# Optimization experiments

Measured on AMD Instinct MI355X. Metric: run time of the kernel, lower is better.

Reference implementation:

```python
import jax, jax.numpy as jnp
import numpy as np

N_QUBITS = 10
N_LAYERS = 4
BATCH = 2048


def setup_inputs() -> dict:
    key = jax.random.key(0)
    k1, k2 = jax.random.split(key)
    x = jax.random.normal(k1, (BATCH, N_QUBITS), dtype=jnp.float32)
    q_params = jax.random.normal(k2, (N_LAYERS * N_QUBITS * 3,), dtype=jnp.float32) * 0.01
    return {"x": x, "q_params": q_params}


def _apply_1q(state, U, wire):
    # state: (B, 2, 2, ..., 2); U: (2, 2) complex. Applies U on `wire`.
    s = jnp.moveaxis(state, wire + 1, -1)
    s = jnp.einsum('...j,ij->...i', s, U)
    return jnp.moveaxis(s, -1, wire + 1)


def _apply_cnot(state, ctrl, tgt):
    # flip target amplitude pair where control bit == 1
    s = jnp.moveaxis(state, (ctrl + 1, tgt + 1), (-2, -1))
    s = jnp.concatenate([s[..., 0:1, :], s[..., 1:2, ::-1]], axis=-2)
    return jnp.moveaxis(s, (-2, -1), (ctrl + 1, tgt + 1))


def _forward(x, q_params):
    B = x.shape[0]
    n, L = N_QUBITS, N_LAYERS
    # --- data-encoding layer: RY(x_i)|0> = [cos(x_i/2), sin(x_i/2)] per qubit ---
    half = 0.5 * x
    amps = jnp.stack([jnp.cos(half), jnp.sin(half)], axis=-1).astype(jnp.complex64)  # (B, n, 2)
    state = amps[:, 0, :]
    for i in range(1, n):  # build product state via successive kron (loop over n_qubits only)
        state = (state[:, :, None] * amps[:, i, None, :]).reshape(B, -1)
    state = state.reshape((B,) + (2,) * n)
    # --- variational gate matrices: per (layer, qubit) fused U = RZ @ RY @ RX ---
    w = q_params.reshape(L, n, 3)
    c, s = jnp.cos(0.5 * w), jnp.sin(0.5 * w)
    cx = c[..., 0].astype(jnp.complex64); sx = s[..., 0].astype(jnp.complex64)
    cy = c[..., 1].astype(jnp.complex64); sy = s[..., 1].astype(jnp.complex64)
    ez = jnp.exp(-0.5j * w[..., 2].astype(jnp.complex64))
    zeros = jnp.zeros_like(ez)
    Urx = jnp.stack([jnp.stack([cx, -1j * sx], -1), jnp.stack([-1j * sx, cx], -1)], -2)  # (L,n,2,2)
    Ury = jnp.stack([jnp.stack([cy, -sy], -1), jnp.stack([sy, cy], -1)], -2)
    Urz = jnp.stack([jnp.stack([ez, zeros], -1), jnp.stack([zeros, jnp.conj(ez)], -1)], -2)
    U = jnp.einsum('lnab,lnbc,lncd->lnad', Urz, Ury, Urx)  # apply order: RX then RY then RZ
    # --- circuit layers ---
    for l in range(L):
        for i in range(n):
            state = _apply_1q(state, U[l, i], i)
        for i in range(n - 1):
            state = _apply_cnot(state, i, i + 1)
    # --- <Z_i> expectation values ---
    p = jnp.abs(state) ** 2  # (B, 2, ..., 2) real probabilities
    evs = []
    for i in range(n):
        axes = tuple(a for a in range(1, n + 1) if a != i + 1)
        pi = jnp.sum(p, axis=axes)  # (B, 2)
        evs.append(pi[:, 0] - pi[:, 1])
    return jnp.stack(evs, axis=-1)  # (B, n_qubits)


def reference(x, q_params):
    return _forward(x, q_params)
```

## Files before the change

### kernel.cpp

```cpp
#include <hip/hip_runtime.h>
#include <math.h>

#define NQ 10
#define NL 4
#define NGATES (NL * NQ)
#define NTHREADS 256
#define WPB 4

typedef float f32x2 __attribute__((ext_vector_type(2)));

#if __has_builtin(__builtin_amdgcn_permlane32_swap)
#define HAVE_PLSWAP 1
#else
#define HAVE_PLSWAP 0
#endif


template<int XM>
__device__ __forceinline__ float exch1(float v, bool selP) {
    if constexpr (XM == 0) return v;
    int x = __float_as_int(v);
    constexpr int low = XM & 31;
    if constexpr (low == 1)      x = __builtin_amdgcn_mov_dpp(x, 0xB1, 0xF, 0xF, true);
    else if constexpr (low == 2) x = __builtin_amdgcn_mov_dpp(x, 0x4E, 0xF, 0xF, true);
    else if constexpr (low == 3) x = __builtin_amdgcn_mov_dpp(x, 0x1B, 0xF, 0xF, true);
    else if constexpr (low != 0) x = __builtin_amdgcn_ds_swizzle(x, (low << 10) | 0x1F);
    if constexpr ((XM & 32) != 0) {
#if HAVE_PLSWAP
        auto r = __builtin_amdgcn_permlane32_swap((unsigned)x, (unsigned)x, false, false);
        x = selP ? (int)r[0] : (int)r[1];
#else
        x = __float_as_int(__shfl_xor(__int_as_float(x), 32, 64));
#endif
    }
    return __int_as_float(x);
}

template<int XM>
__device__ __forceinline__ f32x2 exch2(f32x2 v, bool selP) {
    f32x2 r;
    r.x = exch1<XM>(v.x, selP);
    r.y = exch1<XM>(v.y, selP);
    return r;
}

__device__ __forceinline__ f32x2 cfma4(f32x2 A, f32x2 st, f32x2 B, f32x2 pst) {
    f32x2 t;
    asm("v_pk_mul_f32 %0, %1, %2 op_sel:[0,0] op_sel_hi:[0,1]\n\t"
        "v_pk_fma_f32 %0, %1, %2, %0 op_sel:[1,1,0] op_sel_hi:[1,0,1] neg_lo:[0,1,0]\n\t"
        "v_pk_fma_f32 %0, %3, %4, %0 op_sel:[0,0,0] op_sel_hi:[0,1,1]\n\t"
        "v_pk_fma_f32 %0, %3, %4, %0 op_sel:[1,1,0] op_sel_hi:[1,0,1] neg_lo:[0,1,0]"
        : "=&v"(t)
        : "v"(A), "v"(st), "v"(B), "v"(pst));
    return t;
}

template<int XM, int XR, int SL, int SR>
__device__ __forceinline__ void gate(f32x2 (&st)[16], const f32x2* g4,
                                     int lane, bool selP) {
    f32x2 u00 = g4[0], u01 = g4[1], u10 = g4[2], u11 = g4[3];
    bool hl = (__popc(lane & SL) & 1) != 0;
    f32x2 A0, B0, A1, B1;
    A0.x = hl ? u11.x : u00.x;  A0.y = hl ? u11.y : u00.y;
    B0.x = hl ? u10.x : u01.x;  B0.y = hl ? u10.y : u01.y;
    A1.x = hl ? u00.x : u11.x;  A1.y = hl ? u00.y : u11.y;
    B1.x = hl ? u01.x : u10.x;  B1.y = hl ? u01.y : u10.y;
    f32x2 pst[16];
    #pragma unroll
    for (int r = 0; r < 16; ++r) pst[r] = exch2<XM>(st[r ^ XR], selP);
    #pragma unroll
    for (int r = 0; r < 16; ++r) {
        const bool p1 = (__builtin_popcount(r & SR) & 1) != 0;
        f32x2 Ar = p1 ? A1 : A0;
        f32x2 Br = p1 ? B1 : B0;
        st[r] = cfma4(Ar, st[r], Br, pst[r]);
    }
}

__device__ __forceinline__ float wht6(float v, int lane, bool selP) {
    float t;
    t = exch1<1>(v, selP);   v = (lane & 1)  ? (t - v) : (v + t);
    t = exch1<2>(v, selP);   v = (lane & 2)  ? (t - v) : (v + t);
    t = exch1<4>(v, selP);   v = (lane & 4)  ? (t - v) : (v + t);
    t = exch1<8>(v, selP);   v = (lane & 8)  ? (t - v) : (v + t);
    t = exch1<16>(v, selP);  v = (lane & 16) ? (t - v) : (v + t);
    t = exch1<32>(v, selP);  v = (lane & 32) ? (t - v) : (v + t);
    return v;
}

__global__ __launch_bounds__(NTHREADS, 2) void qlayer_kernel(
    const float* __restrict__ x,
    const float* __restrict__ qp,
    float* __restrict__ out,
    int B)
{
    __shared__ f32x2 su[NGATES][4];

    const int t = threadIdx.x;
    if (t < NGATES) {
        float w0 = qp[t * 3 + 0], w1 = qp[t * 3 + 1], w2 = qp[t * 3 + 2];
        float cx = __cosf(0.5f * w0), sx = __sinf(0.5f * w0);
        float cy = __cosf(0.5f * w1), sy = __sinf(0.5f * w1);
        float er = __cosf(0.5f * w2), ei = -__sinf(0.5f * w2);
        float m00r =  cy * cx, m00i =  sy * sx;
        float m01r = -sy * cx, m01i = -cy * sx;
        float m10r =  sy * cx, m10i = -cy * sx;
        float m11r =  cy * cx, m11i = -sy * sx;
        f32x2 v;
        v.x = er * m00r - ei * m00i;  v.y = er * m00i + ei * m00r;  su[t][0] = v;
        v.x = er * m01r - ei * m01i;  v.y = er * m01i + ei * m01r;  su[t][1] = v;
        v.x = er * m10r + ei * m10i;  v.y = er * m10i - ei * m10r;  su[t][2] = v;
        v.x = er * m11r + ei * m11i;  v.y = er * m11i - ei * m11r;  su[t][3] = v;
    }
    __syncthreads();

    const int lane = t & 63;
    const int b = blockIdx.x * WPB + (t >> 6);
    if (b >= B) return;

    bool selP = false;
#if HAVE_PLSWAP
    {
        auto pr = __builtin_amdgcn_permlane32_swap((unsigned)lane, (unsigned)lane, false, false);
        selP = ((int)pr[0] == (lane ^ 32));
    }
#endif

    float c[NQ], s[NQ];
    #pragma unroll
    for (int q = 0; q < NQ; ++q) {
        float h = 0.5f * x[b * NQ + q];
        c[q] = __cosf(h);  s[q] = __sinf(h);
    }

    float lf = ((lane & 16) ? s[0] : c[0]) * ((lane & 8) ? s[1] : c[1]) *
               ((lane &  4) ? s[2] : c[2]) * ((lane & 32) ? s[7] : c[7]) *
               ((lane &  2) ? s[8] : c[8]) * ((lane &  1) ? s[9] : c[9]);
    f32x2 st[16];
    #pragma unroll
    for (int r = 0; r < 16; ++r) {
        st[r].x = lf * ((r & 8) ? s[3] : c[3]) * ((r & 4) ? s[4] : c[4]) *
                       ((r & 2) ? s[5] : c[5]) * ((r & 1) ? s[6] : c[6]);
        st[r].y = 0.0f;
    }

#define GATE(L, Q, XM, XR, SLm, SRm) \
    gate<XM, XR, SLm, SRm>(st, &su[(L)*NQ+(Q)][0], lane, selP);

    GATE(0,0, 16,0, 16,0)  GATE(0,1, 8,0, 8,0)   GATE(0,2, 4,0, 4,0)
    GATE(0,3, 0,8, 0,8)    GATE(0,4, 0,4, 0,4)   GATE(0,5, 0,2, 0,2)
    GATE(0,6, 0,1, 0,1)    GATE(0,7, 32,0, 32,0) GATE(0,8, 2,0, 2,0)
    GATE(0,9, 1,0, 1,0)
    GATE(1,0, 24,0, 16,0)  GATE(1,1, 12,0, 24,0) GATE(1,2, 4,8, 28,0)
    GATE(1,3, 0,12, 28,8)  GATE(1,4, 0,6, 28,12) GATE(1,5, 0,3, 28,14)
    GATE(1,6, 32,1, 28,15) GATE(1,7, 34,0, 60,15) GATE(1,8, 3,0, 62,15)
    GATE(1,9, 1,0, 63,15)
    GATE(2,0, 20,0, 16,0)  GATE(2,1, 8,8, 8,0)   GATE(2,2, 4,4, 20,0)
    GATE(2,3, 0,10, 8,8)   GATE(2,4, 0,5, 20,4)  GATE(2,5, 32,2, 8,10)
    GATE(2,6, 2,1, 20,5)   GATE(2,7, 33,0, 40,10) GATE(2,8, 2,0, 22,5)
    GATE(2,9, 1,0, 41,10)
    GATE(3,0, 28,8, 16,0)  GATE(3,1, 12,12, 24,0) GATE(3,2, 4,14, 12,0)
    GATE(3,3, 0,15, 4,8)   GATE(3,4, 32,7, 16,12) GATE(3,5, 34,3, 24,6)
    GATE(3,6, 35,1, 12,3)  GATE(3,7, 35,0, 36,9)  GATE(3,8, 3,0, 50,12)
    GATE(3,9, 1,0, 27,6)
#undef GATE

    float p[16];
    #pragma unroll
    for (int r = 0; r < 16; ++r) p[r] = st[r].x * st[r].x + st[r].y * st[r].y;
    float a[8], f8 = 0.0f;
    #pragma unroll
    for (int r = 0; r < 8; ++r) { a[r] = p[r] + p[r + 8]; f8 += p[r] - p[r + 8]; }
    float c4[4], f4 = 0.0f;
    #pragma unroll
    for (int r = 0; r < 4; ++r) { c4[r] = a[r] + a[r + 4]; f4 += a[r] - a[r + 4]; }
    float e2[2], f2 = 0.0f;
    #pragma unroll
    for (int r = 0; r < 2; ++r) { e2[r] = c4[r] + c4[r + 2]; f2 += c4[r] - c4[r + 2]; }
    float P  = e2[0] + e2[1];
    float f1 = e2[0] - e2[1];

    float wP = wht6(P,  lane, selP);
    float w8 = wht6(f8, lane, selP);
    float w4 = wht6(f4, lane, selP);
    float w2 = wht6(f2, lane, selP);
    float w1 = wht6(f1, lane, selP);

    float* o = out + b * NQ;
    if (lane == 16) { o[0] = wP; o[4] = w4; }
    if (lane ==  8) { o[1] = wP; o[5] = w2; }
    if (lane ==  4) { o[2] = wP; o[6] = w1; }
    if (lane ==  0) { o[3] = w8; }
    if (lane == 32) { o[7] = w8; }
    if (lane == 18) { o[8] = w4; }
    if (lane ==  9) { o[9] = w2; }
}

extern "C" void kernel_launch(void* const* d_in, const int* in_sizes, int n_in,
                              void* d_out, int out_size, void* d_ws, size_t ws_size,
                              hipStream_t stream) {
    const float* x  = (const float*)d_in[0];
    const float* qp = (const float*)d_in[1];
    float* out = (float*)d_out;
    const int B = in_sizes[0] / NQ;
    const int blocks = (B + WPB - 1) / WPB;
    qlayer_kernel<<<blocks, NTHREADS, 0, stream>>>(x, qp, out, B);
}
```

Measured before the change: 75.43 us.

## Process two batch elements per wavefront to interleave gate chains and amortize coefficient loads

Each wavefront now simulates two batch samples at once, applying every gate to both state vectors in an interleaved way. It also preloads a whole layer of gate coefficients from LDS into registers once per layer. This raises instruction-level parallelism so the DPP/swizzle exchange latency and FMA dependency chains of the two states can overlap, and it halves LDS coefficient reads per sample. In exchange register pressure roughly doubles (launch bounds relaxed to 1), and the grid has half as many waves (256 blocks), which may reduce occupancy and latency hiding.

Result: slower. 80.74 us (+7.0%).

```diff
diff --git a/kernel.cpp b/kernel.cpp
--- a/kernel.cpp
+++ b/kernel.cpp
@@ -5,7 +5,8 @@
 #define NL 4
 #define NGATES (NL * NQ)
 #define NTHREADS 256
-#define WPB 4
+#define BPW 2
+#define WAVES 4
 
 typedef float f32x2 __attribute__((ext_vector_type(2)));
 
@@ -56,24 +57,27 @@
 }
 
 template<int XM, int XR, int SL, int SR>
-__device__ __forceinline__ void gate(f32x2 (&st)[16], const f32x2* g4,
-                                     int lane, bool selP) {
-    f32x2 u00 = g4[0], u01 = g4[1], u10 = g4[2], u11 = g4[3];
-    bool hl = (__popc(lane & SL) & 1) != 0;
+__device__ __forceinline__ void gate2(f32x2 (&sa)[16], f32x2 (&sb)[16],
+                                      const f32x2 (&g4)[4], int lane, bool selP) {
+    bool hl = (SL != 0) && ((__popc(lane & SL) & 1) != 0);
     f32x2 A0, B0, A1, B1;
-    A0.x = hl ? u11.x : u00.x;  A0.y = hl ? u11.y : u00.y;
-    B0.x = hl ? u10.x : u01.x;  B0.y = hl ? u10.y : u01.y;
-    A1.x = hl ? u00.x : u11.x;  A1.y = hl ? u00.y : u11.y;
-    B1.x = hl ? u01.x : u10.x;  B1.y = hl ? u01.y : u10.y;
-    f32x2 pst[16];
-    #pragma unroll
-    for (int r = 0; r < 16; ++r) pst[r] = exch2<XM>(st[r ^ XR], selP);
+    A0.x = hl ? g4[3].x : g4[0].x;  A0.y = hl ? g4[3].y : g4[0].y;
+    B0.x = hl ? g4[2].x : g4[1].x;  B0.y = hl ? g4[2].y : g4[1].y;
+    A1.x = hl ? g4[0].x : g4[3].x;  A1.y = hl ? g4[0].y : g4[3].y;
+    B1.x = hl ? g4[1].x : g4[2].x;  B1.y = hl ? g4[1].y : g4[2].y;
+    f32x2 pa[16], pb[16];
+    #pragma unroll
+    for (int r = 0; r < 16; ++r) {
+        pa[r] = exch2<XM>(sa[r ^ XR], selP);
+        pb[r] = exch2<XM>(sb[r ^ XR], selP);
+    }
     #pragma unroll
     for (int r = 0; r < 16; ++r) {
         const bool p1 = (__builtin_popcount(r & SR) & 1) != 0;
         f32x2 Ar = p1 ? A1 : A0;
         f32x2 Br = p1 ? B1 : B0;
-        st[r] = cfma4(Ar, st[r], Br, pst[r]);
+        sa[r] = cfma4(Ar, sa[r], Br, pa[r]);
+        sb[r] = cfma4(Ar, sb[r], Br, pb[r]);
     }
 }
 
@@ -88,7 +92,58 @@
     return v;
 }
 
-__global__ __launch_bounds__(NTHREADS, 2) void qlayer_kernel(
+__device__ __forceinline__ void init_state(const float* __restrict__ x, int b,
+                                           int lane, f32x2 (&st)[16]) {
+    float c[NQ], s[NQ];
+    #pragma unroll
+    for (int q = 0; q < NQ; ++q) {
+        float h = 0.5f * x[b * NQ + q];
+        c[q] = __cosf(h);  s[q] = __sinf(h);
+    }
+    float lf = ((lane & 16) ? s[0] : c[0]) * ((lane & 8) ? s[1] : c[1]) *
+               ((lane &  4) ? s[2] : c[2]) * ((lane & 32) ? s[7] : c[7]) *
+               ((lane &  2) ? s[8] : c[8]) * ((lane &  1) ? s[9] : c[9]);
+    #pragma unroll
+    for (int r = 0; r < 16; ++r) {
+        st[r].x = lf * ((r & 8) ? s[3] : c[3]) * ((r & 4) ? s[4] : c[4]) *
+                       ((r & 2) ? s[5] : c[5]) * ((r & 1) ? s[6] : c[6]);
+        st[r].y = 0.0f;
+    }
+}
+
+__device__ __forceinline__ void epilogue(const f32x2 (&st)[16], int lane,
+                                         bool selP, float* __restrict__ o) {
+    float p[16];
+    #pragma unroll
+    for (int r = 0; r < 16; ++r) p[r] = st[r].x * st[r].x + st[r].y * st[r].y;
+    float a[8], f8 = 0.0f;
+    #pragma unroll
+    for (int r = 0; r < 8; ++r) { a[r] = p[r] + p[r + 8]; f8 += p[r] - p[r + 8]; }
+    float c4[4], f4 = 0.0f;
+    #pragma unroll
+    for (int r = 0; r < 4; ++r) { c4[r] = a[r] + a[r + 4]; f4 += a[r] - a[r + 4]; }
+    float e2[2], f2 = 0.0f;
+    #pragma unroll
+    for (int r = 0; r < 2; ++r) { e2[r] = c4[r] + c4[r + 2]; f2 += c4[r] - c4[r + 2]; }
+    float P  = e2[0] + e2[1];
+    float f1 = e2[0] - e2[1];
+
+    float wP = wht6(P,  lane, selP);
+    float w8 = wht6(f8, lane, selP);
+    float w4 = wht6(f4, lane, selP);
+    float w2 = wht6(f2, lane, selP);
+    float w1 = wht6(f1, lane, selP);
+
+    if (lane == 16) { o[0] = wP; o[4] = w4; }
+    if (lane ==  8) { o[1] = wP; o[5] = w2; }
+    if (lane ==  4) { o[2] = wP; o[6] = w1; }
+    if (lane ==  0) { o[3] = w8; }
+    if (lane == 32) { o[7] = w8; }
+    if (lane == 18) { o[8] = w4; }
+    if (lane ==  9) { o[9] = w2; }
+}
+
+__global__ __launch_bounds__(NTHREADS, 1) void qlayer_kernel(
     const float* __restrict__ x,
     const float* __restrict__ qp,
     float* __restrict__ out,
@@ -115,8 +170,9 @@
     __syncthreads();
 
     const int lane = t & 63;
-    const int b = blockIdx.x * WPB + (t >> 6);
-    if (b >= B) return;
+    const int wave = t >> 6;
+    const int b0 = (blockIdx.x * WAVES + wave) * BPW;
+    if (b0 >= B) return;
 
     bool selP = false;
 #if HAVE_PLSWAP
@@ -126,74 +182,53 @@
     }
 #endif
 
-    float c[NQ], s[NQ];
-    #pragma unroll
-    for (int q = 0; q < NQ; ++q) {
-        float h = 0.5f * x[b * NQ + q];
-        c[q] = __cosf(h);  s[q] = __sinf(h);
-    }
-
-    float lf = ((lane & 16) ? s[0] : c[0]) * ((lane & 8) ? s[1] : c[1]) *
-               ((lane &  4) ? s[2] : c[2]) * ((lane & 32) ? s[7] : c[7]) *
-               ((lane &  2) ? s[8] : c[8]) * ((lane &  1) ? s[9] : c[9]);
-    f32x2 st[16];
-    #pragma unroll
-    for (int r = 0; r < 16; ++r) {
-        st[r].x = lf * ((r & 8) ? s[3] : c[3]) * ((r & 4) ? s[4] : c[4]) *
-                       ((r & 2) ? s[5] : c[5]) * ((r & 1) ? s[6] : c[6]);
-        st[r].y = 0.0f;
-    }
-
-#define GATE(L, Q, XM, XR, SLm, SRm) \
-    gate<XM, XR, SLm, SRm>(st, &su[(L)*NQ+(Q)][0], lane, selP);
-
-    GATE(0,0, 16,0, 16,0)  GATE(0,1, 8,0, 8,0)   GATE(0,2, 4,0, 4,0)
-    GATE(0,3, 0,8, 0,8)    GATE(0,4, 0,4, 0,4)   GATE(0,5, 0,2, 0,2)
-    GATE(0,6, 0,1, 0,1)    GATE(0,7, 32,0, 32,0) GATE(0,8, 2,0, 2,0)
-    GATE(0,9, 1,0, 1,0)
-    GATE(1,0, 24,0, 16,0)  GATE(1,1, 12,0, 24,0) GATE(1,2, 4,8, 28,0)
-    GATE(1,3, 0,12, 28,8)  GATE(1,4, 0,6, 28,12) GATE(1,5, 0,3, 28,14)
-    GATE(1,6, 32,1, 28,15) GATE(1,7, 34,0, 60,15) GATE(1,8, 3,0, 62,15)
-    GATE(1,9, 1,0, 63,15)
-    GATE(2,0, 20,0, 16,0)  GATE(2,1, 8,8, 8,0)   GATE(2,2, 4,4, 20,0)
-    GATE(2,3, 0,10, 8,8)   GATE(2,4, 0,5, 20,4)  GATE(2,5, 32,2, 8,10)
-    GATE(2,6, 2,1, 20,5)   GATE(2,7, 33,0, 40,10) GATE(2,8, 2,0, 22,5)
-    GATE(2,9, 1,0, 41,10)
-    GATE(3,0, 28,8, 16,0)  GATE(3,1, 12,12, 24,0) GATE(3,2, 4,14, 12,0)
-    GATE(3,3, 0,15, 4,8)   GATE(3,4, 32,7, 16,12) GATE(3,5, 34,3, 24,6)
-    GATE(3,6, 35,1, 12,3)  GATE(3,7, 35,0, 36,9)  GATE(3,8, 3,0, 50,12)
-    GATE(3,9, 1,0, 27,6)
+    f32x2 sa[16], sb[16];
+    init_state(x, b0, lane, sa);
+    init_state(x, (b0 + 1 < B) ? b0 + 1 : b0, lane, sb);
+
+#define PREFETCH(L)                                                   \
+    f32x2 cf[NQ][4];                                                  \
+    _Pragma("unroll")                                                 \
+    for (int q = 0; q < NQ; ++q) {                                    \
+        cf[q][0] = su[(L)*NQ + q][0];  cf[q][1] = su[(L)*NQ + q][1];  \
+        cf[q][2] = su[(L)*NQ + q][2];  cf[q][3] = su[(L)*NQ + q][3];  \
+    }
+#define GATE(Q, XM, XR, SLm, SRm) \
+    gate2<XM, XR, SLm, SRm>(sa, sb, cf[Q], lane, selP);
+
+    {
+        PREFETCH(0)
+        GATE(0, 16,0, 16,0)  GATE(1, 8,0, 8,0)    GATE(2, 4,0, 4,0)
+        GATE(3, 0,8, 0,8)    GATE(4, 0,4, 0,4)    GATE(5, 0,2, 0,2)
+        GATE(6, 0,1, 0,1)    GATE(7, 32,0, 32,0)  GATE(8, 2,0, 2,0)
+        GATE(9, 1,0, 1,0)
+    }
+    {
+        PREFETCH(1)
+        GATE(0, 24,0, 16,0)  GATE(1, 12,0, 24,0)  GATE(2, 4,8, 28,0)
+        GATE(3, 0,12, 28,8)  GATE(4, 0,6, 28,12)  GATE(5, 0,3, 28,14)
+        GATE(6, 32,1, 28,15) GATE(7, 34,0, 60,15) GATE(8, 3,0, 62,15)
+        GATE(9, 1,0, 63,15)
+    }
+    {
+        PREFETCH(2)
+        GATE(0, 20,0, 16,0)  GATE(1, 8,8, 8,0)    GATE(2, 4,4, 20,0)
+        GATE(3, 0,10, 8,8)   GATE(4, 0,5, 20,4)   GATE(5, 32,2, 8,10)
+        GATE(6, 2,1, 20,5)   GATE(7, 33,0, 40,10) GATE(8, 2,0, 22,5)
+        GATE(9, 1,0, 41,10)
+    }
+    {
+        PREFETCH(3)
+        GATE(0, 28,8, 16,0)  GATE(1, 12,12, 24,0) GATE(2, 4,14, 12,0)
+        GATE(3, 0,15, 4,8)   GATE(4, 32,7, 16,12) GATE(5, 34,3, 24,6)
+        GATE(6, 35,1, 12,3)  GATE(7, 35,0, 36,9)  GATE(8, 3,0, 50,12)
+        GATE(9, 1,0, 27,6)
+    }
 #undef GATE
-
-    float p[16];
-    #pragma unroll
-    for (int r = 0; r < 16; ++r) p[r] = st[r].x * st[r].x + st[r].y * st[r].y;
-    float a[8], f8 = 0.0f;
-    #pragma unroll
-    for (int r = 0; r < 8; ++r) { a[r] = p[r] + p[r + 8]; f8 += p[r] - p[r + 8]; }
-    float c4[4], f4 = 0.0f;
-    #pragma unroll
-    for (int r = 0; r < 4; ++r) { c4[r] = a[r] + a[r + 4]; f4 += a[r] - a[r + 4]; }
-    float e2[2], f2 = 0.0f;
-    #pragma unroll
-    for (int r = 0; r < 2; ++r) { e2[r] = c4[r] + c4[r + 2]; f2 += c4[r] - c4[r + 2]; }
-    float P  = e2[0] + e2[1];
-    float f1 = e2[0] - e2[1];
-
-    float wP = wht6(P,  lane, selP);
-    float w8 = wht6(f8, lane, selP);
-    float w4 = wht6(f4, lane, selP);
-    float w2 = wht6(f2, lane, selP);
-    float w1 = wht6(f1, lane, selP);
-
-    float* o = out + b * NQ;
-    if (lane == 16) { o[0] = wP; o[4] = w4; }
-    if (lane ==  8) { o[1] = wP; o[5] = w2; }
-    if (lane ==  4) { o[2] = wP; o[6] = w1; }
-    if (lane ==  0) { o[3] = w8; }
-    if (lane == 32) { o[7] = w8; }
-    if (lane == 18) { o[8] = w4; }
-    if (lane ==  9) { o[9] = w2; }
+#undef PREFETCH
+
+    epilogue(sa, lane, selP, out + b0 * NQ);
+    if (b0 + 1 < B) epilogue(sb, lane, selP, out + (b0 + 1) * NQ);
 }
 
 extern "C" void kernel_launch(void* const* d_in, const int* in_sizes, int n_in,
@@ -203,6 +238,7 @@
     const float* qp = (const float*)d_in[1];
     float* out = (float*)d_out;
     const int B = in_sizes[0] / NQ;
-    const int blocks = (B + WPB - 1) / WPB;
+    const int bpb = WAVES * BPW;
+    const int blocks = (B + bpb - 1) / bpb;
     qlayer_kernel<<<blocks, NTHREADS, 0, stream>>>(x, qp, out, B);
 }
```
